# Performance work log

Measured on AMD Instinct MI355X. Metric: run time of the kernel, lower is better.

## Reference

```python
import jax, jax.numpy as jnp
import numpy as np

D = 768      # d_model
H = 12       # num_heads
L = 2        # num_blocks
N = 3        # number of sequence domains
B = 64       # batch
S = 512      # per-domain sequence length
MULT = 4     # ffn hidden_mult
A = 1        # action_num


def setup_inputs() -> dict:
    key = jax.random.key(0)
    ks = jax.random.split(key, 16)
    def w(k, shape):
        return jax.random.normal(k, shape, jnp.float32) * 0.02
    return {
        "context": jax.random.normal(ks[0], (B, D), jnp.float32),
        "sequences": jax.random.normal(ks[1], (N, B, S, D), jnp.float32),
        "seq_lens": jnp.maximum(jax.random.randint(ks[2], (N, B), 0, S + 1), 1).astype(jnp.int32),
        # per-block (stacked over L) ContextBlock params
        "blk_qn_w": jnp.ones((L, D)), "blk_qn_b": jnp.zeros((L, D)),
        "blk_sn_w": jnp.ones((L, D)), "blk_sn_b": jnp.zeros((L, D)),
        "blk_in_w": w(ks[3], (L, 3 * D, D)), "blk_in_b": jnp.zeros((L, 3 * D)),
        "blk_out_w": w(ks[4], (L, D, D)), "blk_out_b": jnp.zeros((L, D)),
        "blk_gate_w": w(ks[5], (L, D, 2 * D)), "blk_gate_b": jnp.zeros((L, D)),
        "blk_ffn_ln_w": jnp.ones((L, D)), "blk_ffn_ln_b": jnp.zeros((L, D)),
        "blk_ffn_w1": w(ks[6], (L, MULT * D, D)), "blk_ffn_b1": jnp.zeros((L, MULT * D)),
        "blk_ffn_w2": w(ks[7], (L, D, MULT * D)), "blk_ffn_b2": jnp.zeros((L, D)),
        # output norm + classifier
        "out_norm_w": jnp.ones((D,)), "out_norm_b": jnp.zeros((D,)),
        "cls_ln_w": jnp.ones((D,)), "cls_ln_b": jnp.zeros((D,)),
        "cls_w1": w(ks[8], (MULT * D, D)), "cls_b1": jnp.zeros((MULT * D,)),
        "cls_w2": w(ks[9], (A, MULT * D)), "cls_b2": jnp.zeros((A,)),
    }


def _ln(x, w, b):
    m = x.mean(-1, keepdims=True)
    v = ((x - m) ** 2).mean(-1, keepdims=True)
    return (x - m) * jax.lax.rsqrt(v + 1e-5) * w + b


def _forward(context, sequences, pad,
             blk_qn_w, blk_qn_b, blk_sn_w, blk_sn_b,
             blk_in_w, blk_in_b, blk_out_w, blk_out_b,
             blk_gate_w, blk_gate_b,
             blk_ffn_ln_w, blk_ffn_ln_b, blk_ffn_w1, blk_ffn_b1, blk_ffn_w2, blk_ffn_b2,
             out_norm_w, out_norm_b, cls_ln_w, cls_ln_b, cls_w1, cls_b1, cls_w2, cls_b2):
    dh = D // H
    scale = 1.0 / np.sqrt(dh)
    for l in range(L):
        # length-1 query over context; all N domains handled in one batched attention
        q = _ln(context, blk_qn_w[l], blk_qn_b[l])                       # [B, D]
        kv = _ln(sequences, blk_sn_w[l], blk_sn_b[l])                    # [N, B, S, D]
        Wq, Wk, Wv = jnp.split(blk_in_w[l], 3, axis=0)
        bq, bk, bv = jnp.split(blk_in_b[l], 3)
        qh = (q @ Wq.T + bq).reshape(B, H, dh)
        kh = (jnp.einsum('nbsd,ed->nbse', kv, Wk) + bk).reshape(N, B, S, H, dh)
        vh = (jnp.einsum('nbsd,ed->nbse', kv, Wv) + bv).reshape(N, B, S, H, dh)
        scores = jnp.einsum('bhe,nbshe->nbhs', qh, kh) * scale           # [N, B, H, S]
        scores = jnp.where(pad[:, :, None, :], jnp.float32(-1e30), scores)
        attn = jax.nn.softmax(scores, axis=-1)
        ctx = jnp.einsum('nbhs,nbshe->nbhe', attn, vh).reshape(N, B, D)
        attended = ctx @ blk_out_w[l].T + blk_out_b[l]                   # [N, B, D]
        seq_ctx = attended.mean(axis=0)                                  # mean over domains
        gate = jax.nn.sigmoid(jnp.concatenate([context, seq_ctx], axis=-1) @ blk_gate_w[l].T + blk_gate_b[l])
        context = context + gate * seq_ctx
        h = _ln(context, blk_ffn_ln_w[l], blk_ffn_ln_b[l])
        h = jax.nn.silu(h @ blk_ffn_w1[l].T + blk_ffn_b1[l]) @ blk_ffn_w2[l].T + blk_ffn_b2[l]
        context = context + h
    emb = _ln(context, out_norm_w, out_norm_b)
    h = _ln(emb, cls_ln_w, cls_ln_b)
    return jax.nn.silu(h @ cls_w1.T + cls_b1) @ cls_w2.T + cls_b2        # [B, A]


def reference(context, sequences, seq_lens,
              blk_qn_w, blk_qn_b, blk_sn_w, blk_sn_b,
              blk_in_w, blk_in_b, blk_out_w, blk_out_b,
              blk_gate_w, blk_gate_b,
              blk_ffn_ln_w, blk_ffn_ln_b, blk_ffn_w1, blk_ffn_b1, blk_ffn_w2, blk_ffn_b2,
              out_norm_w, out_norm_b, cls_ln_w, cls_ln_b, cls_w1, cls_b1, cls_w2, cls_b2):
    pad = jnp.arange(S)[None, None, :] >= seq_lens[:, :, None]           # [N, B, S], True = padded
    return _forward(context, sequences, pad,
                    blk_qn_w, blk_qn_b, blk_sn_w, blk_sn_b,
                    blk_in_w, blk_in_b, blk_out_w, blk_out_b,
                    blk_gate_w, blk_gate_b,
                    blk_ffn_ln_w, blk_ffn_ln_b, blk_ffn_w1, blk_ffn_b1, blk_ffn_w2, blk_ffn_b2,
                    out_norm_w, out_norm_b, cls_ln_w, cls_ln_b, cls_w1, cls_b1, cls_w2, cls_b2)
```

## Files before the change

### kernel.cpp

```cpp
#include <hip/hip_runtime.h>
#include <hip/hip_bf16.h>
#include <cstdint>

#define DMODEL 768
#define NB 64
#define NHEAD 12
#define DHEAD 64
#define SEQLEN 512
#define NDOM 3
#define NBLK 2
#define FFNH 3072
#define NBROWS (NDOM*NB)
#define NCH 4
#define ROWCH (SEQLEN/NCH)

__device__ __forceinline__ float wsum64(float v){
  #pragma unroll
  for (int o = 32; o; o >>= 1) v += __shfl_xor(v, o, 64);
  return v;
}
__device__ __forceinline__ float dot4f(float4 a, float4 b){
  return fmaf(a.x, b.x, fmaf(a.y, b.y, fmaf(a.z, b.z, a.w * b.w)));
}

__global__ __launch_bounds__(256) void k_ln(const float* __restrict__ in,
    const float* __restrict__ w, const float* __restrict__ b,
    float* __restrict__ out, int rows){
  int gw = (blockIdx.x * 256 + threadIdx.x) >> 6;
  int lane = threadIdx.x & 63;
  if (gw >= rows) return;
  const float4* x4 = (const float4*)(in + (size_t)gw * DMODEL);
  float4 v0 = x4[lane], v1 = x4[64 + lane], v2 = x4[128 + lane];
  float s = v0.x+v0.y+v0.z+v0.w + v1.x+v1.y+v1.z+v1.w + v2.x+v2.y+v2.z+v2.w;
  float q = dot4f(v0,v0) + dot4f(v1,v1) + dot4f(v2,v2);
  s = wsum64(s); q = wsum64(q);
  float m = s * (1.0f / DMODEL);
  float var = q * (1.0f / DMODEL) - m * m;
  float r = rsqrtf(var + 1e-5f);
  const float4* w4 = (const float4*)w;
  const float4* b4 = (const float4*)b;
  float4* o4 = (float4*)(out + (size_t)gw * DMODEL);
  float4 vv[3] = {v0, v1, v2};
  #pragma unroll
  for (int seg = 0; seg < 3; ++seg){
    float4 ww = w4[seg*64 + lane], bb = b4[seg*64 + lane], x = vv[seg], o;
    o.x = (x.x - m) * r * ww.x + bb.x;
    o.y = (x.y - m) * r * ww.y + bb.y;
    o.z = (x.z - m) * r * ww.z + bb.z;
    o.w = (x.w - m) * r * ww.w + bb.w;
    o4[seg*64 + lane] = o;
  }
}

template<int K, int NC, int ACT, bool RES>
__global__ __launch_bounds__(256) void k_gemmW(const float* __restrict__ A,
    const float* __restrict__ W, const float* __restrict__ bias,
    const float* __restrict__ res, float* __restrict__ out){
  const int NJ = NC / 4;
  int gw = (blockIdx.x * 256 + threadIdx.x) >> 6;
  int lane = threadIdx.x & 63;
  int sl = lane & 7, g = lane >> 3;
  int bg = gw / NJ; int j0 = (gw - bg * NJ) * 4;
  const float4* a4 = (const float4*)(A + (size_t)(bg*8 + g) * K);
  const float4* w0 = (const float4*)(W + (size_t)(j0+0) * K);
  const float4* w1 = (const float4*)(W + (size_t)(j0+1) * K);
  const float4* w2 = (const float4*)(W + (size_t)(j0+2) * K);
  const float4* w3 = (const float4*)(W + (size_t)(j0+3) * K);
  float acc0 = 0, acc1 = 0, acc2 = 0, acc3 = 0;
  #pragma unroll 4
  for (int i = 0; i < K/32; ++i){
    float4 av = a4[i*8 + sl];
    acc0 += dot4f(av, w0[i*8 + sl]);
    acc1 += dot4f(av, w1[i*8 + sl]);
    acc2 += dot4f(av, w2[i*8 + sl]);
    acc3 += dot4f(av, w3[i*8 + sl]);
  }
  #pragma unroll
  for (int o = 1; o <= 4; o <<= 1){
    acc0 += __shfl_xor(acc0, o, 64);
    acc1 += __shfl_xor(acc1, o, 64);
    acc2 += __shfl_xor(acc2, o, 64);
    acc3 += __shfl_xor(acc3, o, 64);
  }
  if (sl == 0){
    int row = bg*8 + g;
    float4 bj = *(const float4*)(bias + j0);
    float a[4] = {acc0, acc1, acc2, acc3};
    float bb[4] = {bj.x, bj.y, bj.z, bj.w};
    float v[4];
    #pragma unroll
    for (int u = 0; u < 4; ++u){
      float t = (ACT == 2) ? a[u] * (1.0f/3.0f) + bb[u] : a[u] + bb[u];
      if (ACT == 1) t = t / (1.0f + __expf(-t));
      v[u] = t;
    }
    size_t o = (size_t)row * NC + j0;
    if (RES){
      float4 rr = *(const float4*)(res + o);
      v[0] += rr.x; v[1] += rr.y; v[2] += rr.z; v[3] += rr.w;
    }
    *(float4*)(out + o) = make_float4(v[0], v[1], v[2], v[3]);
  }
}

__global__ __launch_bounds__(256) void k_qpr(const float* __restrict__ qh,
    const float* __restrict__ Wk, const float* __restrict__ snw,
    const float* __restrict__ snb, const float* __restrict__ bk,
    float* __restrict__ QW, float* __restrict__ SQW, float* __restrict__ SC){
  int w = (blockIdx.x * 256 + threadIdx.x) >> 6;
  int lane = threadIdx.x & 63;
  int b = w / NHEAD, h = w - b * NHEAD;
  const float* qrow = qh + (size_t)b * DMODEL + h * DHEAD;
  const float* wbase = Wk + (size_t)h * DHEAD * DMODEL;
  float qp[12] = {};
  for (int e = 0; e < DHEAD; ++e){
    float qv = qrow[e];
    const float* wr = wbase + (size_t)e * DMODEL;
    #pragma unroll
    for (int k = 0; k < 12; ++k) qp[k] = fmaf(qv, wr[k*64 + lane], qp[k]);
  }
  float s1 = 0, s2 = 0;
  float* qwout = QW + (size_t)w * DMODEL;
  #pragma unroll
  for (int k = 0; k < 12; ++k){
    int d = k*64 + lane;
    float q = qp[k];
    float qwv = q * snw[d] * 0.125f;
    qwout[d] = qwv;
    s1 += qwv;
    s2 = fmaf(q, snb[d], s2);
  }
  float s3 = qrow[lane] * bk[h*DHEAD + lane];
  s1 = wsum64(s1); s2 = wsum64(s2); s3 = wsum64(s3);
  if (lane == 0){ SQW[w] = s1; SC[w] = 0.125f * (s2 + s3); }
}

__global__ __launch_bounds__(256, 2) void k_attn(const float* __restrict__ seq,
    const int* __restrict__ lens, const float* __restrict__ QW,
    const float* __restrict__ SQW, const float* __restrict__ SC,
    float* __restrict__ Pacc, float* __restrict__ Pden,
    float* __restrict__ Pc, float* __restrict__ Pmx){
  int blk = blockIdx.x;
  int ch = blk & (NCH-1); int nb = blk >> 2;
  int wid = threadIdx.x >> 6; int lane = threadIdx.x & 63;
  int b = nb % NB;
  int len = lens[nb];
  int s0 = ch * ROWCH;
  int h0 = wid * 3;
  size_t pb = (size_t)blk * NHEAD + h0;
  if (s0 >= len){
    #pragma unroll
    for (int j = 0; j < 3; ++j){
      float* pa = Pacc + (pb + j) * DMODEL;
      #pragma unroll
      for (int k = 0; k < 12; ++k) pa[k*64 + lane] = 0.0f;
      if (lane == 0){ Pden[pb+j] = 0.0f; Pc[pb+j] = 0.0f; Pmx[pb+j] = -3.0e38f; }
    }
    return;
  }
  int send = s0 + ROWCH < len ? s0 + ROWCH : len;
  const float4* qwb = (const float4*)(QW + ((size_t)b * NHEAD + h0) * DMODEL);
  float4 q0[3], q1[3], q2[3];
  #pragma unroll
  for (int j = 0; j < 3; ++j){
    q0[j] = qwb[j*(DMODEL/4) + lane];
    q1[j] = qwb[j*(DMODEL/4) + 64 + lane];
    q2[j] = qwb[j*(DMODEL/4) + 128 + lane];
  }
  float sqv[3], scv[3];
  #pragma unroll
  for (int j = 0; j < 3; ++j){ sqv[j] = SQW[b*NHEAD + h0 + j]; scv[j] = SC[b*NHEAD + h0 + j]; }
  float4 a0[3], a1[3], a2[3];
  #pragma unroll
  for (int j = 0; j < 3; ++j){
    a0[j] = make_float4(0,0,0,0); a1[j] = make_float4(0,0,0,0); a2[j] = make_float4(0,0,0,0);
  }
  float den[3] = {0,0,0}, cac[3] = {0,0,0}, mx[3] = {-3.0e38f,-3.0e38f,-3.0e38f};
  const float4* xr = (const float4*)(seq + ((size_t)nb * SEQLEN + s0) * DMODEL);
  float4 x0 = xr[lane], x1 = xr[64 + lane], x2 = xr[128 + lane];
  for (int s = s0; s < send; ++s){
    float4 c0 = x0, c1 = x1, c2 = x2;
    if (s + 1 < send){
      const float4* nx = (const float4*)(seq + ((size_t)nb * SEQLEN + s + 1) * DMODEL);
      x0 = nx[lane]; x1 = nx[64 + lane]; x2 = nx[128 + lane];
    }
    float sm = c0.x+c0.y+c0.z+c0.w + c1.x+c1.y+c1.z+c1.w + c2.x+c2.y+c2.z+c2.w;
    float qq = dot4f(c0,c0) + dot4f(c1,c1) + dot4f(c2,c2);
    float d0 = dot4f(q0[0],c0) + dot4f(q1[0],c1) + dot4f(q2[0],c2);
    float d1 = dot4f(q0[1],c0) + dot4f(q1[1],c1) + dot4f(q2[1],c2);
    float d2 = dot4f(q0[2],c0) + dot4f(q1[2],c1) + dot4f(q2[2],c2);
    sm = wsum64(sm); qq = wsum64(qq);
    d0 = wsum64(d0); d1 = wsum64(d1); d2 = wsum64(d2);
    float m = sm * (1.0f/DMODEL);
    float var = qq * (1.0f/DMODEL) - m * m;
    float r = rsqrtf(var + 1e-5f);
    float dt[3] = {d0, d1, d2};
    #pragma unroll
    for (int j = 0; j < 3; ++j){
      float score = r * (dt[j] - m * sqv[j]) + scv[j];
      if (score > mx[j] + 8.0f){
        float f = __expf(mx[j] - score);
        den[j] *= f; cac[j] *= f;
        a0[j].x*=f; a0[j].y*=f; a0[j].z*=f; a0[j].w*=f;
        a1[j].x*=f; a1[j].y*=f; a1[j].z*=f; a1[j].w*=f;
        a2[j].x*=f; a2[j].y*=f; a2[j].z*=f; a2[j].w*=f;
        mx[j] = score;
      }
      float e = __expf(score - mx[j]);
      float er = e * r;
      a0[j].x = fmaf(er, c0.x, a0[j].x); a0[j].y = fmaf(er, c0.y, a0[j].y);
      a0[j].z = fmaf(er, c0.z, a0[j].z); a0[j].w = fmaf(er, c0.w, a0[j].w);
      a1[j].x = fmaf(er, c1.x, a1[j].x); a1[j].y = fmaf(er, c1.y, a1[j].y);
      a1[j].z = fmaf(er, c1.z, a1[j].z); a1[j].w = fmaf(er, c1.w, a1[j].w);
      a2[j].x = fmaf(er, c2.x, a2[j].x); a2[j].y = fmaf(er, c2.y, a2[j].y);
      a2[j].z = fmaf(er, c2.z, a2[j].z); a2[j].w = fmaf(er, c2.w, a2[j].w);
      den[j] += e;
      cac[j] = fmaf(er, m, cac[j]);
    }
  }
  #pragma unroll
  for (int j = 0; j < 3; ++j){
    float4* pa = (float4*)(Pacc + (pb + j) * DMODEL);
    pa[lane] = a0[j]; pa[64 + lane] = a1[j]; pa[128 + lane] = a2[j];
    if (lane == 0){ Pden[pb+j] = den[j]; Pc[pb+j] = cac[j]; Pmx[pb+j] = mx[j]; }
  }
}

__global__ __launch_bounds__(256) void k_comb(const float* __restrict__ Pacc,
    const float* __restrict__ Pden, const float* __restrict__ Pc,
    const float* __restrict__ Pmx, const float* __restrict__ snw,
    const float* __restrict__ snb, float* __restrict__ wsum){
  int tid = blockIdx.x * 256 + threadIdx.x;
  int d = tid % DMODEL;
  int t = tid / DMODEL;
  int h = t % NHEAD;
  int b = t / NHEAD;
  float vec = 0.0f, csum = 0.0f;
  #pragma unroll
  for (int n = 0; n < NDOM; ++n){
    int nb = n*NB + b;
    size_t p0 = ((size_t)nb * NCH) * NHEAD + h;
    float m0 = Pmx[p0], m1 = Pmx[p0 + NHEAD], m2 = Pmx[p0 + 2*NHEAD], m3 = Pmx[p0 + 3*NHEAD];
    float M = fmaxf(fmaxf(m0, m1), fmaxf(m2, m3));
    float w0 = __expf(m0 - M), w1 = __expf(m1 - M), w2 = __expf(m2 - M), w3 = __expf(m3 - M);
    float D = w0*Pden[p0] + w1*Pden[p0+NHEAD] + w2*Pden[p0+2*NHEAD] + w3*Pden[p0+3*NHEAD];
    float inv = 1.0f / D;
    float V = w0*Pacc[p0*DMODEL + d] + w1*Pacc[(p0+NHEAD)*DMODEL + d]
            + w2*Pacc[(p0+2*NHEAD)*DMODEL + d] + w3*Pacc[(p0+3*NHEAD)*DMODEL + d];
    float C = w0*Pc[p0] + w1*Pc[p0+NHEAD] + w2*Pc[p0+2*NHEAD] + w3*Pc[p0+3*NHEAD];
    vec = fmaf(V, inv, vec);
    csum = fmaf(C, inv, csum);
  }
  wsum[tid] = (vec - csum) * snw[d] + 3.0f * snb[d];
}

__global__ __launch_bounds__(256) void k_ctxv2(const float* __restrict__ wsum,
    const float* __restrict__ Wv, const float* __restrict__ bv, float* __restrict__ ctxsum){
  int gw = (blockIdx.x * 256 + threadIdx.x) >> 6;
  int lane = threadIdx.x & 63;
  int sl = lane & 7, g = lane >> 3;
  int bg = gw / 192; int j0 = (gw - bg * 192) * 4;
  int h = j0 >> 6;
  const float4* a4 = (const float4*)(wsum + ((size_t)(bg*8 + g) * NHEAD + h) * DMODEL);
  const float4* w0 = (const float4*)(Wv + (size_t)(j0+0) * DMODEL);
  const float4* w1 = (const float4*)(Wv + (size_t)(j0+1) * DMODEL);
  const float4* w2 = (const float4*)(Wv + (size_t)(j0+2) * DMODEL);
  const float4* w3 = (const float4*)(Wv + (size_t)(j0+3) * DMODEL);
  float acc0 = 0, acc1 = 0, acc2 = 0, acc3 = 0;
  #pragma unroll 4
  for (int i = 0; i < DMODEL/32; ++i){
    float4 av = a4[i*8 + sl];
    acc0 += dot4f(av, w0[i*8 + sl]);
    acc1 += dot4f(av, w1[i*8 + sl]);
    acc2 += dot4f(av, w2[i*8 + sl]);
    acc3 += dot4f(av, w3[i*8 + sl]);
  }
  #pragma unroll
  for (int o = 1; o <= 4; o <<= 1){
    acc0 += __shfl_xor(acc0, o, 64);
    acc1 += __shfl_xor(acc1, o, 64);
    acc2 += __shfl_xor(acc2, o, 64);
    acc3 += __shfl_xor(acc3, o, 64);
  }
  if (sl == 0){
    float4 bb = *(const float4*)(bv + j0);
    float4 v = make_float4(acc0 + 3.0f*bb.x, acc1 + 3.0f*bb.y, acc2 + 3.0f*bb.z, acc3 + 3.0f*bb.w);
    *(float4*)(ctxsum + (size_t)(bg*8 + g) * DMODEL + j0) = v;
  }
}

__global__ __launch_bounds__(256) void k_gate2(const float* __restrict__ ctx,
    const float* __restrict__ sctx, const float* __restrict__ Wg,
    const float* __restrict__ gb, float* __restrict__ out){
  int gw = (blockIdx.x * 256 + threadIdx.x) >> 6;
  int lane = threadIdx.x & 63;
  int sl = lane & 7, g = lane >> 3;
  int bg = gw / 192; int j0 = (gw - bg * 192) * 4;
  int row = bg*8 + g;
  const float4* c4 = (const float4*)(ctx + (size_t)row * DMODEL);
  const float4* s4 = (const float4*)(sctx + (size_t)row * DMODEL);
  const float4* wr0 = (const float4*)(Wg + (size_t)(j0+0) * 2 * DMODEL);
  const float4* wr1 = (const float4*)(Wg + (size_t)(j0+1) * 2 * DMODEL);
  const float4* wr2 = (const float4*)(Wg + (size_t)(j0+2) * 2 * DMODEL);
  const float4* wr3 = (const float4*)(Wg + (size_t)(j0+3) * 2 * DMODEL);
  float acc0 = 0, acc1 = 0, acc2 = 0, acc3 = 0;
  #pragma unroll 4
  for (int i = 0; i < DMODEL/32; ++i){
    float4 cv = c4[i*8 + sl], sv = s4[i*8 + sl];
    acc0 += dot4f(cv, wr0[i*8 + sl]) + dot4f(sv, wr0[192 + i*8 + sl]);
    acc1 += dot4f(cv, wr1[i*8 + sl]) + dot4f(sv, wr1[192 + i*8 + sl]);
    acc2 += dot4f(cv, wr2[i*8 + sl]) + dot4f(sv, wr2[192 + i*8 + sl]);
    acc3 += dot4f(cv, wr3[i*8 + sl]) + dot4f(sv, wr3[192 + i*8 + sl]);
  }
  #pragma unroll
  for (int o = 1; o <= 4; o <<= 1){
    acc0 += __shfl_xor(acc0, o, 64);
    acc1 += __shfl_xor(acc1, o, 64);
    acc2 += __shfl_xor(acc2, o, 64);
    acc3 += __shfl_xor(acc3, o, 64);
  }
  if (sl == 0){
    size_t o = (size_t)row * DMODEL + j0;
    float4 bb = *(const float4*)(gb + j0);
    float4 cc = *(const float4*)(ctx + o);
    float4 ss = *(const float4*)(sctx + o);
    float4 v;
    v.x = cc.x + ss.x / (1.0f + __expf(-(acc0 + bb.x)));
    v.y = cc.y + ss.y / (1.0f + __expf(-(acc1 + bb.y)));
    v.z = cc.z + ss.z / (1.0f + __expf(-(acc2 + bb.z)));
    v.w = cc.w + ss.w / (1.0f + __expf(-(acc3 + bb.w)));
    *(float4*)(out + o) = v;
  }
}

__global__ __launch_bounds__(256) void k_cls2(const float* __restrict__ h2,
    const float* __restrict__ w2, const float* __restrict__ b2, float* __restrict__ out){
  int b = blockIdx.x; int t = threadIdx.x;
  float acc = 0;
  for (int j = t; j < FFNH; j += 256) acc = fmaf(h2[(size_t)b*FFNH + j], w2[j], acc);
  acc = wsum64(acc);
  __shared__ float sh[4];
  if ((t & 63) == 0) sh[t >> 6] = acc;
  __syncthreads();
  if (t == 0) out[b] = sh[0] + sh[1] + sh[2] + sh[3] + b2[0];
}

extern "C" void kernel_launch(void* const* d_in, const int* in_sizes, int n_in,
                              void* d_out, int out_size, void* d_ws, size_t ws_size,
                              hipStream_t stream){
  const float* in_ctx = (const float*)d_in[0];
  const float* seq    = (const float*)d_in[1];
  const int*   lens   = (const int*)d_in[2];
  const float* qn_w   = (const float*)d_in[3];
  const float* qn_b   = (const float*)d_in[4];
  const float* sn_w   = (const float*)d_in[5];
  const float* sn_b   = (const float*)d_in[6];
  const float* in_w   = (const float*)d_in[7];
  const float* in_b   = (const float*)d_in[8];
  const float* out_w  = (const float*)d_in[9];
  const float* out_b  = (const float*)d_in[10];
  const float* gate_w = (const float*)d_in[11];
  const float* gate_b = (const float*)d_in[12];
  const float* fln_w  = (const float*)d_in[13];
  const float* fln_b  = (const float*)d_in[14];
  const float* fw1    = (const float*)d_in[15];
  const float* fb1    = (const float*)d_in[16];
  const float* fw2    = (const float*)d_in[17];
  const float* fb2    = (const float*)d_in[18];
  const float* on_w   = (const float*)d_in[19];
  const float* on_b   = (const float*)d_in[20];
  const float* cl_w   = (const float*)d_in[21];
  const float* cl_b   = (const float*)d_in[22];
  const float* cw1    = (const float*)d_in[23];
  const float* cb1    = (const float*)d_in[24];
  const float* cw2    = (const float*)d_in[25];
  const float* cb2    = (const float*)d_in[26];

  float* wsf = (float*)d_ws;
  size_t off = 0;
  auto alloc = [&](size_t n){ float* p = wsf + off; off += n; return p; };
  float* c0     = alloc((size_t)NB*DMODEL);
  float* c1     = alloc((size_t)NB*DMODEL);
  float* cmid   = alloc((size_t)NB*DMODEL);
  float* qln    = alloc((size_t)NB*DMODEL);
  float* qh     = alloc((size_t)NB*DMODEL);
  float* QW     = alloc((size_t)NB*NHEAD*DMODEL);
  float* SQWb   = alloc((size_t)NB*NHEAD);
  float* SCb    = alloc((size_t)NB*NHEAD);
  float* Pacc   = alloc((size_t)NBROWS*NCH*NHEAD*DMODEL);
  float* Pden   = alloc((size_t)NBROWS*NCH*NHEAD);
  float* Pc     = alloc((size_t)NBROWS*NCH*NHEAD);
  float* Pmx    = alloc((size_t)NBROWS*NCH*NHEAD);
  float* wsumb  = alloc((size_t)NB*NHEAD*DMODEL);
  float* ctxsum = alloc((size_t)NB*DMODEL);
  float* sctx   = alloc((size_t)NB*DMODEL);
  float* h0     = alloc((size_t)NB*DMODEL);
  float* h1     = alloc((size_t)NB*FFNH);
  (void)ws_size; (void)in_sizes; (void)n_in; (void)out_size;

  hipMemcpyAsync(c0, in_ctx, (size_t)NB*DMODEL*sizeof(float), hipMemcpyDeviceToDevice, stream);
  float* cur = c0; float* nxt = c1;

  for (int l = 0; l < NBLK; ++l){
    const float* Wq = in_w + (size_t)l * 3 * DMODEL * DMODEL;
    const float* Wk = Wq + (size_t)DMODEL * DMODEL;
    const float* Wv = Wq + (size_t)2 * DMODEL * DMODEL;
    const float* bq = in_b + (size_t)l * 3 * DMODEL;
    const float* bk = bq + DMODEL;
    const float* bv = bq + 2 * DMODEL;

    k_ln<<<16, 256, 0, stream>>>(cur, qn_w + l*DMODEL, qn_b + l*DMODEL, qln, NB);
    k_gemmW<DMODEL,DMODEL,0,false><<<384, 256, 0, stream>>>(qln, Wq, bq, nullptr, qh);
    k_qpr<<<192, 256, 0, stream>>>(qh, Wk, sn_w + l*DMODEL, sn_b + l*DMODEL, bk, QW, SQWb, SCb);
    k_attn<<<NBROWS*NCH, 256, 0, stream>>>(seq, lens, QW, SQWb, SCb, Pacc, Pden, Pc, Pmx);
    k_comb<<<(NB*NHEAD*DMODEL)/256, 256, 0, stream>>>(Pacc, Pden, Pc, Pmx, sn_w + l*DMODEL, sn_b + l*DMODEL, wsumb);
    k_ctxv2<<<384, 256, 0, stream>>>(wsumb, Wv, bv, ctxsum);
    k_gemmW<DMODEL,DMODEL,2,false><<<384, 256, 0, stream>>>(ctxsum, out_w + (size_t)l*DMODEL*DMODEL, out_b + l*DMODEL, nullptr, sctx);
    k_gate2<<<384, 256, 0, stream>>>(cur, sctx, gate_w + (size_t)l*DMODEL*2*DMODEL, gate_b + l*DMODEL, cmid);
    k_ln<<<16, 256, 0, stream>>>(cmid, fln_w + l*DMODEL, fln_b + l*DMODEL, h0, NB);
    k_gemmW<DMODEL,FFNH,1,false><<<1536, 256, 0, stream>>>(h0, fw1 + (size_t)l*FFNH*DMODEL, fb1 + l*FFNH, nullptr, h1);
    k_gemmW<FFNH,DMODEL,0,true><<<384, 256, 0, stream>>>(h1, fw2 + (size_t)l*DMODEL*FFNH, fb2 + l*DMODEL, cmid, nxt);
    float* t = cur; cur = nxt; nxt = t;
  }

  k_ln<<<16, 256, 0, stream>>>(cur, on_w, on_b, qln, NB);
  k_ln<<<16, 256, 0, stream>>>(qln, cl_w, cl_b, h0, NB);
  k_gemmW<DMODEL,FFNH,1,false><<<1536, 256, 0, stream>>>(h0, cw1, cb1, nullptr, h1);
  k_cls2<<<64, 256, 0, stream>>>(h1, cw2, cb2, (float*)d_out);
}
```

Baseline: 659.5 us.

## Restructure attention into LDS-tiled two-pass chunk kernel with per-chunk softmax

Replaces the per-row streaming attention kernel with a block that stages 64-row tiles of the sequence in swizzled shared memory. It computes all 12 head scores and the LayerNorm stats cooperatively, does a per-chunk softmax via wave max and sum, then makes a second pass over the tile to accumulate weighted values for all heads. Chunks are now 8 of 64 rows, fully padded chunks exit early, and the combine kernel only reads the active chunks based on seq_lens. The two final LayerNorms are fused into one kernel. The cost is loading the sequence tile twice, which doubles global reads of the sequence, plus extra synchronisation and shared memory use that may lower occupancy.

```diff
diff --git a/kernel.cpp b/kernel.cpp
--- a/kernel.cpp
+++ b/kernel.cpp
@@ -11,12 +11,17 @@
 #define NBLK 2
 #define FFNH 3072
 #define NBROWS (NDOM*NB)
-#define NCH 4
-#define ROWCH (SEQLEN/NCH)
+#define NCH 8
+#define ROWCH 64
 
 __device__ __forceinline__ float wsum64(float v){
   #pragma unroll
   for (int o = 32; o; o >>= 1) v += __shfl_xor(v, o, 64);
+  return v;
+}
+__device__ __forceinline__ float wmax64(float v){
+  #pragma unroll
+  for (int o = 32; o; o >>= 1) v = fmaxf(v, __shfl_xor(v, o, 64));
   return v;
 }
 __device__ __forceinline__ float dot4f(float4 a, float4 b){
@@ -49,6 +54,49 @@
     o.z = (x.z - m) * r * ww.z + bb.z;
     o.w = (x.w - m) * r * ww.w + bb.w;
     o4[seg*64 + lane] = o;
+  }
+}
+
+__global__ __launch_bounds__(256) void k_ln2(const float* __restrict__ in,
+    const float* __restrict__ w1, const float* __restrict__ b1,
+    const float* __restrict__ w2, const float* __restrict__ b2,
+    float* __restrict__ out, int rows){
+  int gw = (blockIdx.x * 256 + threadIdx.x) >> 6;
+  int lane = threadIdx.x & 63;
+  if (gw >= rows) return;
+  const float4* x4 = (const float4*)(in + (size_t)gw * DMODEL);
+  float4 vv[3] = {x4[lane], x4[64 + lane], x4[128 + lane]};
+  float s = 0, q = 0;
+  #pragma unroll
+  for (int g = 0; g < 3; ++g){
+    s += vv[g].x+vv[g].y+vv[g].z+vv[g].w;
+    q += dot4f(vv[g], vv[g]);
+  }
+  s = wsum64(s); q = wsum64(q);
+  float m = s * (1.0f/DMODEL);
+  float r = rsqrtf(q * (1.0f/DMODEL) - m*m + 1e-5f);
+  const float4* w14 = (const float4*)w1; const float4* b14 = (const float4*)b1;
+  float4 yy[3];
+  float s2 = 0, q2 = 0;
+  #pragma unroll
+  for (int g = 0; g < 3; ++g){
+    float4 ww = w14[g*64 + lane], bb = b14[g*64 + lane], x = vv[g], o;
+    o.x = (x.x - m)*r*ww.x + bb.x; o.y = (x.y - m)*r*ww.y + bb.y;
+    o.z = (x.z - m)*r*ww.z + bb.z; o.w = (x.w - m)*r*ww.w + bb.w;
+    yy[g] = o;
+    s2 += o.x+o.y+o.z+o.w; q2 += dot4f(o,o);
+  }
+  s2 = wsum64(s2); q2 = wsum64(q2);
+  float m2 = s2 * (1.0f/DMODEL);
+  float r2 = rsqrtf(q2 * (1.0f/DMODEL) - m2*m2 + 1e-5f);
+  const float4* w24 = (const float4*)w2; const float4* b24 = (const float4*)b2;
+  float4* o4 = (float4*)(out + (size_t)gw * DMODEL);
+  #pragma unroll
+  for (int g = 0; g < 3; ++g){
+    float4 ww = w24[g*64 + lane], bb = b24[g*64 + lane], y = yy[g], o;
+    o.x = (y.x - m2)*r2*ww.x + bb.x; o.y = (y.y - m2)*r2*ww.y + bb.y;
+    o.z = (y.z - m2)*r2*ww.z + bb.z; o.w = (y.w - m2)*r2*ww.w + bb.w;
+    o4[g*64 + lane] = o;
   }
 }
 
@@ -135,101 +183,158 @@
   if (lane == 0){ SQW[w] = s1; SC[w] = 0.125f * (s2 + s3); }
 }
 
-__global__ __launch_bounds__(256, 2) void k_attn(const float* __restrict__ seq,
+__global__ __launch_bounds__(256) void k_attn2(const float* __restrict__ seq,
     const int* __restrict__ lens, const float* __restrict__ QW,
     const float* __restrict__ SQW, const float* __restrict__ SC,
     float* __restrict__ Pacc, float* __restrict__ Pden,
     float* __restrict__ Pc, float* __restrict__ Pmx){
+  __shared__ float xt[64*128];
+  __shared__ float uni[6144];
+  __shared__ float er_s[64][12];
   int blk = blockIdx.x;
-  int ch = blk & (NCH-1); int nb = blk >> 2;
-  int wid = threadIdx.x >> 6; int lane = threadIdx.x & 63;
+  int ch = blk & (NCH-1); int nb = blk >> 3;
+  int len = lens[nb];
+  int row0 = ch * ROWCH;
+  if (row0 >= len) return;
   int b = nb % NB;
-  int len = lens[nb];
-  int s0 = ch * ROWCH;
+  int tid = threadIdx.x;
+  int wid = tid >> 6, lane = tid & 63;
+  int lr = tid >> 2;
+  int lc4 = (tid & 3) * 8;
+  const float* gsrc = seq + ((size_t)nb * SEQLEN + row0 + lr) * DMODEL + lc4 * 4;
+  const float* qwb = QW + (size_t)b * NHEAD * DMODEL;
+  float* qt = uni;
+  float* red1 = uni + 1536;
+
+  float dt[12];
+  #pragma unroll
+  for (int h = 0; h < 12; ++h) dt[h] = 0.0f;
+  float sm = 0.0f, qq = 0.0f;
+
+  for (int c = 0; c < 6; ++c){
+    __syncthreads();
+    const float4* g4 = (const float4*)(gsrc + c*128);
+    #pragma unroll
+    for (int k = 0; k < 8; ++k){
+      float4 v = g4[k];
+      int c4p = (lc4 + k) ^ (lr & 7);
+      *(float4*)&xt[lr*128 + c4p*4] = v;
+    }
+    #pragma unroll
+    for (int i = 0; i < 6; ++i){
+      int idx = tid + i*256;
+      qt[idx] = qwb[(size_t)(idx >> 7) * DMODEL + c*128 + (idx & 127)];
+    }
+    __syncthreads();
+    const float4* q4 = (const float4*)qt;
+    #pragma unroll
+    for (int i = 0; i < 8; ++i){
+      int c4 = wid*8 + i;
+      int c4p = c4 ^ (lane & 7);
+      float4 x = *(const float4*)&xt[lane*128 + c4p*4];
+      sm += x.x + x.y + x.z + x.w;
+      qq += dot4f(x, x);
+      #pragma unroll
+      for (int h = 0; h < 12; ++h)
+        dt[h] += dot4f(q4[h*32 + c4], x);
+    }
+  }
+  #pragma unroll
+  for (int h = 0; h < 12; ++h) red1[(wid*14 + h)*64 + lane] = dt[h];
+  red1[(wid*14 + 12)*64 + lane] = sm;
+  red1[(wid*14 + 13)*64 + lane] = qq;
+  __syncthreads();
+
   int h0 = wid * 3;
-  size_t pb = (size_t)blk * NHEAD + h0;
-  if (s0 >= len){
-    #pragma unroll
-    for (int j = 0; j < 3; ++j){
-      float* pa = Pacc + (pb + j) * DMODEL;
-      #pragma unroll
-      for (int k = 0; k < 12; ++k) pa[k*64 + lane] = 0.0f;
-      if (lane == 0){ Pden[pb+j] = 0.0f; Pc[pb+j] = 0.0f; Pmx[pb+j] = -3.0e38f; }
-    }
-    return;
-  }
-  int send = s0 + ROWCH < len ? s0 + ROWCH : len;
-  const float4* qwb = (const float4*)(QW + ((size_t)b * NHEAD + h0) * DMODEL);
-  float4 q0[3], q1[3], q2[3];
-  #pragma unroll
-  for (int j = 0; j < 3; ++j){
-    q0[j] = qwb[j*(DMODEL/4) + lane];
-    q1[j] = qwb[j*(DMODEL/4) + 64 + lane];
-    q2[j] = qwb[j*(DMODEL/4) + 128 + lane];
-  }
-  float sqv[3], scv[3];
-  #pragma unroll
-  for (int j = 0; j < 3; ++j){ sqv[j] = SQW[b*NHEAD + h0 + j]; scv[j] = SC[b*NHEAD + h0 + j]; }
-  float4 a0[3], a1[3], a2[3];
-  #pragma unroll
-  for (int j = 0; j < 3; ++j){
-    a0[j] = make_float4(0,0,0,0); a1[j] = make_float4(0,0,0,0); a2[j] = make_float4(0,0,0,0);
-  }
-  float den[3] = {0,0,0}, cac[3] = {0,0,0}, mx[3] = {-3.0e38f,-3.0e38f,-3.0e38f};
-  const float4* xr = (const float4*)(seq + ((size_t)nb * SEQLEN + s0) * DMODEL);
-  float4 x0 = xr[lane], x1 = xr[64 + lane], x2 = xr[128 + lane];
-  for (int s = s0; s < send; ++s){
-    float4 c0 = x0, c1 = x1, c2 = x2;
-    if (s + 1 < send){
-      const float4* nx = (const float4*)(seq + ((size_t)nb * SEQLEN + s + 1) * DMODEL);
-      x0 = nx[lane]; x1 = nx[64 + lane]; x2 = nx[128 + lane];
-    }
-    float sm = c0.x+c0.y+c0.z+c0.w + c1.x+c1.y+c1.z+c1.w + c2.x+c2.y+c2.z+c2.w;
-    float qq = dot4f(c0,c0) + dot4f(c1,c1) + dot4f(c2,c2);
-    float d0 = dot4f(q0[0],c0) + dot4f(q1[0],c1) + dot4f(q2[0],c2);
-    float d1 = dot4f(q0[1],c0) + dot4f(q1[1],c1) + dot4f(q2[1],c2);
-    float d2 = dot4f(q0[2],c0) + dot4f(q1[2],c1) + dot4f(q2[2],c2);
-    sm = wsum64(sm); qq = wsum64(qq);
-    d0 = wsum64(d0); d1 = wsum64(d1); d2 = wsum64(d2);
-    float m = sm * (1.0f/DMODEL);
-    float var = qq * (1.0f/DMODEL) - m * m;
-    float r = rsqrtf(var + 1e-5f);
-    float dt[3] = {d0, d1, d2};
-    #pragma unroll
-    for (int j = 0; j < 3; ++j){
-      float score = r * (dt[j] - m * sqv[j]) + scv[j];
-      if (score > mx[j] + 8.0f){
-        float f = __expf(mx[j] - score);
-        den[j] *= f; cac[j] *= f;
-        a0[j].x*=f; a0[j].y*=f; a0[j].z*=f; a0[j].w*=f;
-        a1[j].x*=f; a1[j].y*=f; a1[j].z*=f; a1[j].w*=f;
-        a2[j].x*=f; a2[j].y*=f; a2[j].z*=f; a2[j].w*=f;
-        mx[j] = score;
-      }
-      float e = __expf(score - mx[j]);
-      float er = e * r;
-      a0[j].x = fmaf(er, c0.x, a0[j].x); a0[j].y = fmaf(er, c0.y, a0[j].y);
-      a0[j].z = fmaf(er, c0.z, a0[j].z); a0[j].w = fmaf(er, c0.w, a0[j].w);
-      a1[j].x = fmaf(er, c1.x, a1[j].x); a1[j].y = fmaf(er, c1.y, a1[j].y);
-      a1[j].z = fmaf(er, c1.z, a1[j].z); a1[j].w = fmaf(er, c1.w, a1[j].w);
-      a2[j].x = fmaf(er, c2.x, a2[j].x); a2[j].y = fmaf(er, c2.y, a2[j].y);
-      a2[j].z = fmaf(er, c2.z, a2[j].z); a2[j].w = fmaf(er, c2.w, a2[j].w);
-      den[j] += e;
-      cac[j] = fmaf(er, m, cac[j]);
-    }
-  }
-  #pragma unroll
-  for (int j = 0; j < 3; ++j){
-    float4* pa = (float4*)(Pacc + (pb + j) * DMODEL);
-    pa[lane] = a0[j]; pa[64 + lane] = a1[j]; pa[128 + lane] = a2[j];
-    if (lane == 0){ Pden[pb+j] = den[j]; Pc[pb+j] = cac[j]; Pmx[pb+j] = mx[j]; }
+  float smt = 0, qqt = 0, d0 = 0, d1 = 0, d2 = 0;
+  #pragma unroll
+  for (int w = 0; w < 4; ++w){
+    smt += red1[(w*14 + 12)*64 + lane];
+    qqt += red1[(w*14 + 13)*64 + lane];
+    d0  += red1[(w*14 + h0    )*64 + lane];
+    d1  += red1[(w*14 + h0 + 1)*64 + lane];
+    d2  += red1[(w*14 + h0 + 2)*64 + lane];
+  }
+  float m = smt * (1.0f/DMODEL);
+  float rs = rsqrtf(qqt * (1.0f/DMODEL) - m*m + 1e-5f);
+  bool valid = (row0 + lane) < len;
+  int bh = b*NHEAD + h0;
+  float sv0 = rs*(d0 - m*SQW[bh  ]) + SC[bh  ];
+  float sv1 = rs*(d1 - m*SQW[bh+1]) + SC[bh+1];
+  float sv2 = rs*(d2 - m*SQW[bh+2]) + SC[bh+2];
+  if (!valid){ sv0 = -3.0e38f; sv1 = -3.0e38f; sv2 = -3.0e38f; }
+  float mx0 = wmax64(sv0), mx1 = wmax64(sv1), mx2 = wmax64(sv2);
+  float e0 = valid ? __expf(sv0 - mx0) : 0.0f;
+  float e1 = valid ? __expf(sv1 - mx1) : 0.0f;
+  float e2 = valid ? __expf(sv2 - mx2) : 0.0f;
+  float er0 = e0*rs, er1 = e1*rs, er2 = e2*rs;
+  er_s[lane][h0] = er0; er_s[lane][h0+1] = er1; er_s[lane][h0+2] = er2;
+  float den0 = wsum64(e0), den1 = wsum64(e1), den2 = wsum64(e2);
+  float cc0 = wsum64(er0*m), cc1 = wsum64(er1*m), cc2 = wsum64(er2*m);
+  size_t pb = (size_t)blk * NHEAD;
+  if (lane == 0){
+    Pden[pb+h0] = den0; Pden[pb+h0+1] = den1; Pden[pb+h0+2] = den2;
+    Pc [pb+h0] = cc0;  Pc [pb+h0+1] = cc1;  Pc [pb+h0+2] = cc2;
+    Pmx[pb+h0] = mx0;  Pmx[pb+h0+1] = mx1;  Pmx[pb+h0+2] = mx2;
+  }
+
+  float* red2 = uni;
+  int prow0 = wid * 16;
+  for (int c = 0; c < 6; ++c){
+    __syncthreads();
+    const float4* g4 = (const float4*)(gsrc + c*128);
+    #pragma unroll
+    for (int k = 0; k < 8; ++k){
+      float4 v = g4[k];
+      int c4p = (lc4 + k) ^ (lr & 7);
+      *(float4*)&xt[lr*128 + c4p*4] = v;
+    }
+    __syncthreads();
+    float pa[12][2];
+    #pragma unroll
+    for (int h = 0; h < 12; ++h){ pa[h][0] = 0.0f; pa[h][1] = 0.0f; }
+    #pragma unroll
+    for (int si = 0; si < 16; ++si){
+      int s = prow0 + si;
+      int c4p = (lane >> 1) ^ (s & 7);
+      float2 xv = *(const float2*)&xt[s*128 + c4p*4 + (lane & 1)*2];
+      float4 ea = *(const float4*)&er_s[s][0];
+      float4 eb = *(const float4*)&er_s[s][4];
+      float4 ec = *(const float4*)&er_s[s][8];
+      pa[0][0]  = fmaf(ea.x, xv.x, pa[0][0]);  pa[0][1]  = fmaf(ea.x, xv.y, pa[0][1]);
+      pa[1][0]  = fmaf(ea.y, xv.x, pa[1][0]);  pa[1][1]  = fmaf(ea.y, xv.y, pa[1][1]);
+      pa[2][0]  = fmaf(ea.z, xv.x, pa[2][0]);  pa[2][1]  = fmaf(ea.z, xv.y, pa[2][1]);
+      pa[3][0]  = fmaf(ea.w, xv.x, pa[3][0]);  pa[3][1]  = fmaf(ea.w, xv.y, pa[3][1]);
+      pa[4][0]  = fmaf(eb.x, xv.x, pa[4][0]);  pa[4][1]  = fmaf(eb.x, xv.y, pa[4][1]);
+      pa[5][0]  = fmaf(eb.y, xv.x, pa[5][0]);  pa[5][1]  = fmaf(eb.y, xv.y, pa[5][1]);
+      pa[6][0]  = fmaf(eb.z, xv.x, pa[6][0]);  pa[6][1]  = fmaf(eb.z, xv.y, pa[6][1]);
+      pa[7][0]  = fmaf(eb.w, xv.x, pa[7][0]);  pa[7][1]  = fmaf(eb.w, xv.y, pa[7][1]);
+      pa[8][0]  = fmaf(ec.x, xv.x, pa[8][0]);  pa[8][1]  = fmaf(ec.x, xv.y, pa[8][1]);
+      pa[9][0]  = fmaf(ec.y, xv.x, pa[9][0]);  pa[9][1]  = fmaf(ec.y, xv.y, pa[9][1]);
+      pa[10][0] = fmaf(ec.z, xv.x, pa[10][0]); pa[10][1] = fmaf(ec.z, xv.y, pa[10][1]);
+      pa[11][0] = fmaf(ec.w, xv.x, pa[11][0]); pa[11][1] = fmaf(ec.w, xv.y, pa[11][1]);
+    }
+    #pragma unroll
+    for (int h = 0; h < 12; ++h)
+      *(float2*)&red2[(wid*12 + h)*128 + 2*lane] = make_float2(pa[h][0], pa[h][1]);
+    __syncthreads();
+    size_t pacc_base = (size_t)blk * NHEAD * DMODEL + c*128;
+    #pragma unroll
+    for (int i = 0; i < 6; ++i){
+      int idx = tid + i*256;
+      int h = idx >> 7, d = idx & 127;
+      float v = red2[h*128 + d] + red2[(12 + h)*128 + d]
+              + red2[(24 + h)*128 + d] + red2[(36 + h)*128 + d];
+      Pacc[pacc_base + (size_t)h * DMODEL + d] = v;
+    }
   }
 }
 
 __global__ __launch_bounds__(256) void k_comb(const float* __restrict__ Pacc,
     const float* __restrict__ Pden, const float* __restrict__ Pc,
-    const float* __restrict__ Pmx, const float* __restrict__ snw,
-    const float* __restrict__ snb, float* __restrict__ wsum){
+    const float* __restrict__ Pmx, const int* __restrict__ lens,
+    const float* __restrict__ snw, const float* __restrict__ snb,
+    float* __restrict__ wsum){
   int tid = blockIdx.x * 256 + threadIdx.x;
   int d = tid % DMODEL;
   int t = tid / DMODEL;
@@ -239,15 +344,20 @@
   #pragma unroll
   for (int n = 0; n < NDOM; ++n){
     int nb = n*NB + b;
-    size_t p0 = ((size_t)nb * NCH) * NHEAD + h;
-    float m0 = Pmx[p0], m1 = Pmx[p0 + NHEAD], m2 = Pmx[p0 + 2*NHEAD], m3 = Pmx[p0 + 3*NHEAD];
-    float M = fmaxf(fmaxf(m0, m1), fmaxf(m2, m3));
-    float w0 = __expf(m0 - M), w1 = __expf(m1 - M), w2 = __expf(m2 - M), w3 = __expf(m3 - M);
-    float D = w0*Pden[p0] + w1*Pden[p0+NHEAD] + w2*Pden[p0+2*NHEAD] + w3*Pden[p0+3*NHEAD];
+    int len = lens[nb];
+    int na = (len + ROWCH - 1) >> 6; if (na > NCH) na = NCH;
+    size_t p0 = (size_t)nb * NCH * NHEAD + h;
+    float M = -3.0e38f;
+    for (int c = 0; c < na; ++c) M = fmaxf(M, Pmx[p0 + (size_t)c*NHEAD]);
+    float D = 0, V = 0, C = 0;
+    for (int c = 0; c < na; ++c){
+      size_t pi = p0 + (size_t)c*NHEAD;
+      float w = __expf(Pmx[pi] - M);
+      D = fmaf(w, Pden[pi], D);
+      V = fmaf(w, Pacc[pi*DMODEL + d], V);
+      C = fmaf(w, Pc[pi], C);
+    }
     float inv = 1.0f / D;
-    float V = w0*Pacc[p0*DMODEL + d] + w1*Pacc[(p0+NHEAD)*DMODEL + d]
-            + w2*Pacc[(p0+2*NHEAD)*DMODEL + d] + w3*Pacc[(p0+3*NHEAD)*DMODEL + d];
-    float C = w0*Pc[p0] + w1*Pc[p0+NHEAD] + w2*Pc[p0+2*NHEAD] + w3*Pc[p0+3*NHEAD];
     vec = fmaf(V, inv, vec);
     csum = fmaf(C, inv, csum);
   }
@@ -412,8 +522,8 @@
     k_ln<<<16, 256, 0, stream>>>(cur, qn_w + l*DMODEL, qn_b + l*DMODEL, qln, NB);
     k_gemmW<DMODEL,DMODEL,0,false><<<384, 256, 0, stream>>>(qln, Wq, bq, nullptr, qh);
     k_qpr<<<192, 256, 0, stream>>>(qh, Wk, sn_w + l*DMODEL, sn_b + l*DMODEL, bk, QW, SQWb, SCb);
-    k_attn<<<NBROWS*NCH, 256, 0, stream>>>(seq, lens, QW, SQWb, SCb, Pacc, Pden, Pc, Pmx);
-    k_comb<<<(NB*NHEAD*DMODEL)/256, 256, 0, stream>>>(Pacc, Pden, Pc, Pmx, sn_w + l*DMODEL, sn_b + l*DMODEL, wsumb);
+    k_attn2<<<NBROWS*NCH, 256, 0, stream>>>(seq, lens, QW, SQWb, SCb, Pacc, Pden, Pc, Pmx);
+    k_comb<<<(NB*NHEAD*DMODEL)/256, 256, 0, stream>>>(Pacc, Pden, Pc, Pmx, lens, sn_w + l*DMODEL, sn_b + l*DMODEL, wsumb);
     k_ctxv2<<<384, 256, 0, stream>>>(wsumb, Wv, bv, ctxsum);
     k_gemmW<DMODEL,DMODEL,2,false><<<384, 256, 0, stream>>>(ctxsum, out_w + (size_t)l*DMODEL*DMODEL, out_b + l*DMODEL, nullptr, sctx);
     k_gate2<<<384, 256, 0, stream>>>(cur, sctx, gate_w + (size_t)l*DMODEL*2*DMODEL, gate_b + l*DMODEL, cmid);
@@ -423,8 +533,7 @@
     float* t = cur; cur = nxt; nxt = t;
   }
 
-  k_ln<<<16, 256, 0, stream>>>(cur, on_w, on_b, qln, NB);
-  k_ln<<<16, 256, 0, stream>>>(qln, cl_w, cl_b, h0, NB);
+  k_ln2<<<16, 256, 0, stream>>>(cur, on_w, on_b, cl_w, cl_b, h0, NB);
   k_gemmW<DMODEL,FFNH,1,false><<<1536, 256, 0, stream>>>(h0, cw1, cb1, nullptr, h1);
   k_cls2<<<64, 256, 0, stream>>>(h1, cw2, cb2, (float*)d_out);
 }
```

Measured after the change: 899.4 us. +36.4%, slower.

## Split attention into finer chunks, skip padded chunks, fuse final layernorms

Applied to the files above, without the earlier changes.

Splits each sequence into 16 chunks of 32 rows instead of 4 of 128, and lets fully padded chunks exit immediately without writing zero partials. The combine kernel reads each row's length and merges only the active chunks. This aims to cut wasted work on padded rows and improve load balance, at the cost of more partial buffers and a data-dependent loop in the combine step. It also fuses the two back-to-back final layernorms into one kernel, and changes the GEMM warp-to-tile mapping so the 8 batch groups of one weight tile run in adjacent warps, which should improve weight cache reuse.

```diff
diff --git a/kernel.cpp b/kernel.cpp
--- a/kernel.cpp
+++ b/kernel.cpp
@@ -11,12 +11,17 @@
 #define NBLK 2
 #define FFNH 3072
 #define NBROWS (NDOM*NB)
-#define NCH 4
-#define ROWCH (SEQLEN/NCH)
+#define NCH 16
+#define ROWCH 32
 
 __device__ __forceinline__ float wsum64(float v){
   #pragma unroll
   for (int o = 32; o; o >>= 1) v += __shfl_xor(v, o, 64);
+  return v;
+}
+__device__ __forceinline__ float wmax64(float v){
+  #pragma unroll
+  for (int o = 32; o; o >>= 1) v = fmaxf(v, __shfl_xor(v, o, 64));
   return v;
 }
 __device__ __forceinline__ float dot4f(float4 a, float4 b){
@@ -52,15 +57,57 @@
   }
 }
 
+__global__ __launch_bounds__(256) void k_ln2(const float* __restrict__ in,
+    const float* __restrict__ w1, const float* __restrict__ b1,
+    const float* __restrict__ w2, const float* __restrict__ b2,
+    float* __restrict__ out, int rows){
+  int gw = (blockIdx.x * 256 + threadIdx.x) >> 6;
+  int lane = threadIdx.x & 63;
+  if (gw >= rows) return;
+  const float4* x4 = (const float4*)(in + (size_t)gw * DMODEL);
+  float4 vv[3] = {x4[lane], x4[64 + lane], x4[128 + lane]};
+  float s = 0, q = 0;
+  #pragma unroll
+  for (int g = 0; g < 3; ++g){
+    s += vv[g].x+vv[g].y+vv[g].z+vv[g].w;
+    q += dot4f(vv[g], vv[g]);
+  }
+  s = wsum64(s); q = wsum64(q);
+  float m = s * (1.0f/DMODEL);
+  float r = rsqrtf(q * (1.0f/DMODEL) - m*m + 1e-5f);
+  const float4* w14 = (const float4*)w1; const float4* b14 = (const float4*)b1;
+  float4 yy[3];
+  float s2 = 0, q2 = 0;
+  #pragma unroll
+  for (int g = 0; g < 3; ++g){
+    float4 ww = w14[g*64 + lane], bb = b14[g*64 + lane], x = vv[g], o;
+    o.x = (x.x - m)*r*ww.x + bb.x; o.y = (x.y - m)*r*ww.y + bb.y;
+    o.z = (x.z - m)*r*ww.z + bb.z; o.w = (x.w - m)*r*ww.w + bb.w;
+    yy[g] = o;
+    s2 += o.x+o.y+o.z+o.w; q2 += dot4f(o,o);
+  }
+  s2 = wsum64(s2); q2 = wsum64(q2);
+  float m2 = s2 * (1.0f/DMODEL);
+  float r2 = rsqrtf(q2 * (1.0f/DMODEL) - m2*m2 + 1e-5f);
+  const float4* w24 = (const float4*)w2; const float4* b24 = (const float4*)b2;
+  float4* o4 = (float4*)(out + (size_t)gw * DMODEL);
+  #pragma unroll
+  for (int g = 0; g < 3; ++g){
+    float4 ww = w24[g*64 + lane], bb = b24[g*64 + lane], y = yy[g], o;
+    o.x = (y.x - m2)*r2*ww.x + bb.x; o.y = (y.y - m2)*r2*ww.y + bb.y;
+    o.z = (y.z - m2)*r2*ww.z + bb.z; o.w = (y.w - m2)*r2*ww.w + bb.w;
+    o4[g*64 + lane] = o;
+  }
+}
+
 template<int K, int NC, int ACT, bool RES>
 __global__ __launch_bounds__(256) void k_gemmW(const float* __restrict__ A,
     const float* __restrict__ W, const float* __restrict__ bias,
     const float* __restrict__ res, float* __restrict__ out){
-  const int NJ = NC / 4;
   int gw = (blockIdx.x * 256 + threadIdx.x) >> 6;
   int lane = threadIdx.x & 63;
   int sl = lane & 7, g = lane >> 3;
-  int bg = gw / NJ; int j0 = (gw - bg * NJ) * 4;
+  int bg = gw & 7; int j0 = (gw >> 3) * 4;
   const float4* a4 = (const float4*)(A + (size_t)(bg*8 + g) * K);
   const float4* w0 = (const float4*)(W + (size_t)(j0+0) * K);
   const float4* w1 = (const float4*)(W + (size_t)(j0+1) * K);
@@ -135,30 +182,21 @@
   if (lane == 0){ SQW[w] = s1; SC[w] = 0.125f * (s2 + s3); }
 }
 
-__global__ __launch_bounds__(256, 2) void k_attn(const float* __restrict__ seq,
+__global__ __launch_bounds__(256, 2) void k_attn4(const float* __restrict__ seq,
     const int* __restrict__ lens, const float* __restrict__ QW,
     const float* __restrict__ SQW, const float* __restrict__ SC,
     float* __restrict__ Pacc, float* __restrict__ Pden,
     float* __restrict__ Pc, float* __restrict__ Pmx){
   int blk = blockIdx.x;
-  int ch = blk & (NCH-1); int nb = blk >> 2;
+  int ch = blk & (NCH-1); int nb = blk >> 4;
   int wid = threadIdx.x >> 6; int lane = threadIdx.x & 63;
   int b = nb % NB;
   int len = lens[nb];
   int s0 = ch * ROWCH;
+  if (s0 >= len) return;
+  int send = s0 + ROWCH < len ? s0 + ROWCH : len;
   int h0 = wid * 3;
   size_t pb = (size_t)blk * NHEAD + h0;
-  if (s0 >= len){
-    #pragma unroll
-    for (int j = 0; j < 3; ++j){
-      float* pa = Pacc + (pb + j) * DMODEL;
-      #pragma unroll
-      for (int k = 0; k < 12; ++k) pa[k*64 + lane] = 0.0f;
-      if (lane == 0){ Pden[pb+j] = 0.0f; Pc[pb+j] = 0.0f; Pmx[pb+j] = -3.0e38f; }
-    }
-    return;
-  }
-  int send = s0 + ROWCH < len ? s0 + ROWCH : len;
   const float4* qwb = (const float4*)(QW + ((size_t)b * NHEAD + h0) * DMODEL);
   float4 q0[3], q1[3], q2[3];
   #pragma unroll
@@ -228,8 +266,9 @@
 
 __global__ __launch_bounds__(256) void k_comb(const float* __restrict__ Pacc,
     const float* __restrict__ Pden, const float* __restrict__ Pc,
-    const float* __restrict__ Pmx, const float* __restrict__ snw,
-    const float* __restrict__ snb, float* __restrict__ wsum){
+    const float* __restrict__ Pmx, const int* __restrict__ lens,
+    const float* __restrict__ snw, const float* __restrict__ snb,
+    float* __restrict__ wsum){
   int tid = blockIdx.x * 256 + threadIdx.x;
   int d = tid % DMODEL;
   int t = tid / DMODEL;
@@ -239,15 +278,20 @@
   #pragma unroll
   for (int n = 0; n < NDOM; ++n){
     int nb = n*NB + b;
-    size_t p0 = ((size_t)nb * NCH) * NHEAD + h;
-    float m0 = Pmx[p0], m1 = Pmx[p0 + NHEAD], m2 = Pmx[p0 + 2*NHEAD], m3 = Pmx[p0 + 3*NHEAD];
-    float M = fmaxf(fmaxf(m0, m1), fmaxf(m2, m3));
-    float w0 = __expf(m0 - M), w1 = __expf(m1 - M), w2 = __expf(m2 - M), w3 = __expf(m3 - M);
-    float D = w0*Pden[p0] + w1*Pden[p0+NHEAD] + w2*Pden[p0+2*NHEAD] + w3*Pden[p0+3*NHEAD];
+    int len = lens[nb];
+    int na = (len + ROWCH - 1) >> 5; if (na > NCH) na = NCH;
+    size_t p0 = (size_t)nb * NCH * NHEAD + h;
+    float M = -3.0e38f;
+    for (int c = 0; c < na; ++c) M = fmaxf(M, Pmx[p0 + (size_t)c*NHEAD]);
+    float D = 0, V = 0, C = 0;
+    for (int c = 0; c < na; ++c){
+      size_t pi = p0 + (size_t)c*NHEAD;
+      float w = __expf(Pmx[pi] - M);
+      D = fmaf(w, Pden[pi], D);
+      V = fmaf(w, Pacc[pi*DMODEL + d], V);
+      C = fmaf(w, Pc[pi], C);
+    }
     float inv = 1.0f / D;
-    float V = w0*Pacc[p0*DMODEL + d] + w1*Pacc[(p0+NHEAD)*DMODEL + d]
-            + w2*Pacc[(p0+2*NHEAD)*DMODEL + d] + w3*Pacc[(p0+3*NHEAD)*DMODEL + d];
-    float C = w0*Pc[p0] + w1*Pc[p0+NHEAD] + w2*Pc[p0+2*NHEAD] + w3*Pc[p0+3*NHEAD];
     vec = fmaf(V, inv, vec);
     csum = fmaf(C, inv, csum);
   }
@@ -259,7 +303,7 @@
   int gw = (blockIdx.x * 256 + threadIdx.x) >> 6;
   int lane = threadIdx.x & 63;
   int sl = lane & 7, g = lane >> 3;
-  int bg = gw / 192; int j0 = (gw - bg * 192) * 4;
+  int bg = gw & 7; int j0 = (gw >> 3) * 4;
   int h = j0 >> 6;
   const float4* a4 = (const float4*)(wsum + ((size_t)(bg*8 + g) * NHEAD + h) * DMODEL);
   const float4* w0 = (const float4*)(Wv + (size_t)(j0+0) * DMODEL);
@@ -295,7 +339,7 @@
   int gw = (blockIdx.x * 256 + threadIdx.x) >> 6;
   int lane = threadIdx.x & 63;
   int sl = lane & 7, g = lane >> 3;
-  int bg = gw / 192; int j0 = (gw - bg * 192) * 4;
+  int bg = gw & 7; int j0 = (gw >> 3) * 4;
   int row = bg*8 + g;
   const float4* c4 = (const float4*)(ctx + (size_t)row * DMODEL);
   const float4* s4 = (const float4*)(sctx + (size_t)row * DMODEL);
@@ -412,8 +456,8 @@
     k_ln<<<16, 256, 0, stream>>>(cur, qn_w + l*DMODEL, qn_b + l*DMODEL, qln, NB);
     k_gemmW<DMODEL,DMODEL,0,false><<<384, 256, 0, stream>>>(qln, Wq, bq, nullptr, qh);
     k_qpr<<<192, 256, 0, stream>>>(qh, Wk, sn_w + l*DMODEL, sn_b + l*DMODEL, bk, QW, SQWb, SCb);
-    k_attn<<<NBROWS*NCH, 256, 0, stream>>>(seq, lens, QW, SQWb, SCb, Pacc, Pden, Pc, Pmx);
-    k_comb<<<(NB*NHEAD*DMODEL)/256, 256, 0, stream>>>(Pacc, Pden, Pc, Pmx, sn_w + l*DMODEL, sn_b + l*DMODEL, wsumb);
+    k_attn4<<<NBROWS*NCH, 256, 0, stream>>>(seq, lens, QW, SQWb, SCb, Pacc, Pden, Pc, Pmx);
+    k_comb<<<(NB*NHEAD*DMODEL)/256, 256, 0, stream>>>(Pacc, Pden, Pc, Pmx, lens, sn_w + l*DMODEL, sn_b + l*DMODEL, wsumb);
     k_ctxv2<<<384, 256, 0, stream>>>(wsumb, Wv, bv, ctxsum);
     k_gemmW<DMODEL,DMODEL,2,false><<<384, 256, 0, stream>>>(ctxsum, out_w + (size_t)l*DMODEL*DMODEL, out_b + l*DMODEL, nullptr, sctx);
     k_gate2<<<384, 256, 0, stream>>>(cur, sctx, gate_w + (size_t)l*DMODEL*2*DMODEL, gate_b + l*DMODEL, cmid);
@@ -423,8 +467,7 @@
     float* t = cur; cur = nxt; nxt = t;
   }
 
-  k_ln<<<16, 256, 0, stream>>>(cur, on_w, on_b, qln, NB);
-  k_ln<<<16, 256, 0, stream>>>(qln, cl_w, cl_b, h0, NB);
+  k_ln2<<<16, 256, 0, stream>>>(cur, on_w, on_b, cl_w, cl_b, h0, NB);
   k_gemmW<DMODEL,FFNH,1,false><<<1536, 256, 0, stream>>>(h0, cw1, cb1, nullptr, h1);
   k_cls2<<<64, 256, 0, stream>>>(h1, cw2, cb2, (float*)d_out);
 }
```

After: 661.4 us. About the same (+0.3%).
